# Kernel optimization log

Hardware: AMD Instinct MI355X
Metric: run time of the kernel (lower is better)

The kernel has to match this reference:

```python
import jax, jax.numpy as jnp
import numpy as np

N, KIN = 400000, 128
K = 64
RADIUS = 0.5
BIG = 1e9  # sentinel distance for invalid (nidx < 0) neighbours


def setup_inputs() -> dict:
    key = jax.random.key(0)
    k1, k2, k3 = jax.random.split(key, 3)
    distances = jax.random.uniform(k1, (N, KIN), dtype=jnp.float32)
    idx = jax.random.randint(k2, (N, KIN), 0, N, dtype=jnp.int32)
    neg = jax.random.uniform(k3, (N, KIN)) < 0.05
    nidx = jnp.where(neg, jnp.int32(-1), idx)
    return {"distances": distances, "nidx": nidx}


def reference(distances, nidx):
    # Push invalid neighbours to the end of the sort order
    tfdist = jnp.where(nidx < 0, jnp.float32(BIG), distances)
    # Per-row ascending sort by masked distance; only the first K are needed
    sorting = jnp.argsort(tfdist, axis=1)[:, :K]  # [N, K]
    snidx = jnp.take_along_axis(nidx, sorting, axis=1)       # [N, K]
    sdist = jnp.take_along_axis(distances, sorting, axis=1)  # [N, K]
    # Radius mask: drop neighbours beyond RADIUS
    beyond = sdist > RADIUS
    snidx = jnp.where(beyond, jnp.int32(-1), snidx)
    sdist = jnp.where(beyond, jnp.float32(0.0), sdist)
    return (sdist, snidx)
```

## Files before the change

kernel.cpp:

```cpp
#include <hip/hip_runtime.h>

#define N_ROWS 400000
#define KIN 128
#define KOUT 64
#define RPW 4
#define WPB 4

typedef unsigned int uint32;
typedef unsigned int v2u __attribute__((ext_vector_type(2)));


template <int CTRL>
__device__ __forceinline__ uint32 dpp32(uint32 k) {
    return (uint32)__builtin_amdgcn_update_dpp(0, (int)k, CTRL, 0xF, 0xF, true);
}
__device__ __forceinline__ uint32 x4swap(uint32 k) {
    uint32 o = (uint32)__builtin_amdgcn_update_dpp((int)k, (int)k, 0x104, 0xF, 0x5, true);
    o = (uint32)__builtin_amdgcn_update_dpp((int)o, (int)k, 0x114, 0xF, 0xA, true);
    return o;
}
__device__ __forceinline__ void pl32pair(uint32 k, uint32& A, uint32& B) {
    const v2u r = __builtin_amdgcn_permlane32_swap(k, k, false, false);
    A = r[0]; B = r[1];
}
#if __has_builtin(__builtin_amdgcn_permlane16_swap)
__device__ __forceinline__ void pl16pair(uint32 k, uint32& A, uint32& B) {
    const v2u r = __builtin_amdgcn_permlane16_swap(k, k, false, false);
    A = r[0]; B = r[1];
}
#else
__device__ __forceinline__ void pl16pair(uint32 k, uint32& A, uint32& B) {
    A = k; B = (uint32)__builtin_amdgcn_ds_swizzle((int)k, 0x401F);
}
#endif
__device__ __forceinline__ uint32 umin32(uint32 a, uint32 b) { return a < b ? a : b; }
__device__ __forceinline__ uint32 med3(uint32 a, uint32 b, uint32 m) {
    uint32 d;
    asm("v_med3_u32 %0, %1, %2, %3" : "=v"(d) : "v"(a), "v"(b), "v"(m));
    return d;
}

#define T_DPP(CTRL, M) { _Pragma("unroll") \
    for (int r_ = 0; r_ < RPW; ++r_) { \
        keyA[r_] = med3(keyA[r_], dpp32<CTRL>(keyA[r_]), M); \
        keyB[r_] = med3(keyB[r_], dpp32<CTRL>(keyB[r_]), M); } }

#define T_X4(M) { _Pragma("unroll") \
    for (int r_ = 0; r_ < RPW; ++r_) { \
        keyA[r_] = med3(keyA[r_], x4swap(keyA[r_]), M); \
        keyB[r_] = med3(keyB[r_], x4swap(keyB[r_]), M); } }

#define T_PL16(M) { _Pragma("unroll") \
    for (int r_ = 0; r_ < RPW; ++r_) { \
        uint32 A0, B0, A1, B1; \
        pl16pair(keyA[r_], A0, B0); pl16pair(keyB[r_], A1, B1); \
        keyA[r_] = med3(A0, B0, M); \
        keyB[r_] = med3(A1, B1, M); } }

#define T_PL32(M) { _Pragma("unroll") \
    for (int r_ = 0; r_ < RPW; ++r_) { \
        uint32 A0, B0, A1, B1; \
        pl32pair(keyA[r_], A0, B0); pl32pair(keyB[r_], A1, B1); \
        keyA[r_] = med3(A0, B0, M); \
        keyB[r_] = med3(A1, B1, M); } }

#define M_DPP(CTRL, M) { _Pragma("unroll") \
    for (int r_ = 0; r_ < RPW; ++r_) { \
        keyA[r_] = med3(keyA[r_], dpp32<CTRL>(keyA[r_]), M); } }
#define M_X4(M) { _Pragma("unroll") \
    for (int r_ = 0; r_ < RPW; ++r_) { \
        keyA[r_] = med3(keyA[r_], x4swap(keyA[r_]), M); } }
#define M_PL16(M) { _Pragma("unroll") \
    for (int r_ = 0; r_ < RPW; ++r_) { \
        uint32 A, B; pl16pair(keyA[r_], A, B); \
        keyA[r_] = med3(A, B, M); } }
#define M_PL32(M) { _Pragma("unroll") \
    for (int r_ = 0; r_ < RPW; ++r_) { \
        uint32 A, B; pl32pair(keyA[r_], A, B); \
        keyA[r_] = med3(A, B, M); } }

#define QP_X1 0xB1
#define QP_X2 0x4E
#define ROR8  0x128

__global__ __launch_bounds__(256) void SortAndSelectNeighbours_kernel(
    const float* __restrict__ distances,
    const int*   __restrict__ nidx,
    float*       __restrict__ out)
{
    __shared__ int s_nidx[WPB][RPW][KIN];

    const int lane = threadIdx.x & 63;
    const int wid  = threadIdx.x >> 6;
    const int row0 = (blockIdx.x * WPB + wid) * RPW;
    const int c0 = 2 * lane;

    float2 dv[RPW];
    int2   nv[RPW];
    #pragma unroll
    for (int r = 0; r < RPW; ++r) {
        const uint32 off = (uint32)(row0 + r) * KIN + (uint32)c0;
        dv[r] = *reinterpret_cast<const float2*>(distances + off);
        nv[r] = *reinterpret_cast<const int2*>(nidx + off);
    }

    uint32 keyA[RPW], keyB[RPW];
    #pragma unroll
    for (int r = 0; r < RPW; ++r) {
        *reinterpret_cast<int2*>(&s_nidx[wid][r][c0]) = nv[r];
        const uint32 k0 = (uint32)(dv[r].x * 16777216.0f);
        const uint32 k1 = (uint32)(dv[r].y * 16777216.0f);
        keyA[r] =  (((k0 << 7) | (uint32)c0)       | ((uint32)nv[r].x & 0x80000000u));
        keyB[r] = ~(((k1 << 7) | (uint32)(c0 + 1)) | ((uint32)nv[r].y & 0x80000000u));
    }

    const uint32 lm = (uint32)lane;
    const uint32 m0 = (uint32)-(int)(lm & 1u);
    const uint32 m1 = (uint32)-(int)((lm >> 1) & 1u);
    const uint32 m2 = (uint32)-(int)((lm >> 2) & 1u);
    const uint32 m3 = (uint32)-(int)((lm >> 3) & 1u);
    const uint32 m4 = (uint32)-(int)((lm >> 4) & 1u);
    const uint32 m5 = (uint32)-(int)((lm >> 5) & 1u);
    const uint32 g01 = m0 ^ m1;
    const uint32 g12 = m1 ^ m2, g02 = m0 ^ m2;
    const uint32 g23 = m2 ^ m3, g13 = m1 ^ m3, g03 = m0 ^ m3;
    const uint32 g34 = m3 ^ m4, g24 = m2 ^ m4, g14 = m1 ^ m4, g04 = m0 ^ m4;
    const uint32 g45 = m4 ^ m5, g35 = m3 ^ m5, g25 = m2 ^ m5, g15 = m1 ^ m5,
                 g05 = m0 ^ m5;

    T_DPP(QP_X1, g01);
    T_DPP(QP_X2, g12); T_DPP(QP_X1, g02);
    T_X4(g23); T_DPP(QP_X2, g13); T_DPP(QP_X1, g03);
    T_DPP(ROR8, g34); T_X4(g24); T_DPP(QP_X2, g14); T_DPP(QP_X1, g04);
    T_PL16(g45); T_DPP(ROR8, g35); T_X4(g25); T_DPP(QP_X2, g15);
    T_DPP(QP_X1, g05);
    T_PL32(m5); T_PL16(m4); T_DPP(ROR8, m3); T_X4(m2); T_DPP(QP_X2, m1);
    T_DPP(QP_X1, m0);

    #pragma unroll
    for (int r = 0; r < RPW; ++r)
        keyA[r] = umin32(keyA[r], ~keyB[r]);

    M_PL32(m5); M_PL16(m4); M_DPP(ROR8, m3); M_X4(m2); M_DPP(QP_X2, m1);
    M_DPP(QP_X1, m0);

    #pragma unroll
    for (int r = 0; r < RPW; ++r) {
        const bool bey = keyA[r] > 0x4000007Fu;
        const float d = (float)(keyA[r] >> 7) * 5.9604644775390625e-8f;
        const int col = (int)(keyA[r] & 127u);
        const int n   = s_nidx[wid][r][col];

        const uint32 od = (uint32)(row0 + r) * KOUT + (uint32)lane;
        out[od] = bey ? 0.0f : d;
        out[(uint32)(N_ROWS * KOUT) + od] = bey ? -1.0f : (float)n;
    }
}

extern "C" void kernel_launch(void* const* d_in, const int* in_sizes, int n_in,
                              void* d_out, int out_size, void* d_ws, size_t ws_size,
                              hipStream_t stream) {
    const float* distances = (const float*)d_in[0];
    const int*   nidx      = (const int*)d_in[1];
    float*       out       = (float*)d_out;

    dim3 grid(N_ROWS / (WPB * RPW));
    dim3 block(256);
    hipLaunchKernelGGL(SortAndSelectNeighbours_kernel, grid, block, 0, stream,
                       distances, nidx, out);
}
```

Before: 115.4 us.

## Use persistent grid-stride waves with register prefetch of next row group

Replaces the one-wave-per-row-group launch with a fixed grid of 2048 blocks whose waves loop over row groups in grid-stride fashion. The loads for the next group are issued before the sorting network runs on the current one, so memory latency overlaps the DPP/permlane compute. This removes per-block launch and setup overhead but doubles the registers held for input data and reduces the number of waves resident at once. Shared-memory reuse across iterations within a wave relies on wave-level lockstep ordering.

```diff
diff --git a/kernel.cpp b/kernel.cpp
--- a/kernel.cpp
+++ b/kernel.cpp
@@ -5,6 +5,9 @@
 #define KOUT 64
 #define RPW 4
 #define WPB 4
+#define G_BLOCKS 2048
+#define TOT_WAVES (G_BLOCKS * WPB)
+#define TOT_WB (N_ROWS / RPW)
 
 typedef unsigned int uint32;
 typedef unsigned int v2u __attribute__((ext_vector_type(2)));
@@ -44,26 +47,20 @@
     for (int r_ = 0; r_ < RPW; ++r_) { \
         keyA[r_] = med3(keyA[r_], dpp32<CTRL>(keyA[r_]), M); \
         keyB[r_] = med3(keyB[r_], dpp32<CTRL>(keyB[r_]), M); } }
-
 #define T_X4(M) { _Pragma("unroll") \
     for (int r_ = 0; r_ < RPW; ++r_) { \
         keyA[r_] = med3(keyA[r_], x4swap(keyA[r_]), M); \
         keyB[r_] = med3(keyB[r_], x4swap(keyB[r_]), M); } }
-
 #define T_PL16(M) { _Pragma("unroll") \
     for (int r_ = 0; r_ < RPW; ++r_) { \
         uint32 A0, B0, A1, B1; \
         pl16pair(keyA[r_], A0, B0); pl16pair(keyB[r_], A1, B1); \
-        keyA[r_] = med3(A0, B0, M); \
-        keyB[r_] = med3(A1, B1, M); } }
-
+        keyA[r_] = med3(A0, B0, M); keyB[r_] = med3(A1, B1, M); } }
 #define T_PL32(M) { _Pragma("unroll") \
     for (int r_ = 0; r_ < RPW; ++r_) { \
         uint32 A0, B0, A1, B1; \
         pl32pair(keyA[r_], A0, B0); pl32pair(keyB[r_], A1, B1); \
-        keyA[r_] = med3(A0, B0, M); \
-        keyB[r_] = med3(A1, B1, M); } }
-
+        keyA[r_] = med3(A0, B0, M); keyB[r_] = med3(A1, B1, M); } }
 #define M_DPP(CTRL, M) { _Pragma("unroll") \
     for (int r_ = 0; r_ < RPW; ++r_) { \
         keyA[r_] = med3(keyA[r_], dpp32<CTRL>(keyA[r_]), M); } }
@@ -72,12 +69,10 @@
         keyA[r_] = med3(keyA[r_], x4swap(keyA[r_]), M); } }
 #define M_PL16(M) { _Pragma("unroll") \
     for (int r_ = 0; r_ < RPW; ++r_) { \
-        uint32 A, B; pl16pair(keyA[r_], A, B); \
-        keyA[r_] = med3(A, B, M); } }
+        uint32 A, B; pl16pair(keyA[r_], A, B); keyA[r_] = med3(A, B, M); } }
 #define M_PL32(M) { _Pragma("unroll") \
     for (int r_ = 0; r_ < RPW; ++r_) { \
-        uint32 A, B; pl32pair(keyA[r_], A, B); \
-        keyA[r_] = med3(A, B, M); } }
+        uint32 A, B; pl32pair(keyA[r_], A, B); keyA[r_] = med3(A, B, M); } }
 
 #define QP_X1 0xB1
 #define QP_X2 0x4E
@@ -92,27 +87,8 @@
 
     const int lane = threadIdx.x & 63;
     const int wid  = threadIdx.x >> 6;
-    const int row0 = (blockIdx.x * WPB + wid) * RPW;
-    const int c0 = 2 * lane;
-
-    float2 dv[RPW];
-    int2   nv[RPW];
-    #pragma unroll
-    for (int r = 0; r < RPW; ++r) {
-        const uint32 off = (uint32)(row0 + r) * KIN + (uint32)c0;
-        dv[r] = *reinterpret_cast<const float2*>(distances + off);
-        nv[r] = *reinterpret_cast<const int2*>(nidx + off);
-    }
-
-    uint32 keyA[RPW], keyB[RPW];
-    #pragma unroll
-    for (int r = 0; r < RPW; ++r) {
-        *reinterpret_cast<int2*>(&s_nidx[wid][r][c0]) = nv[r];
-        const uint32 k0 = (uint32)(dv[r].x * 16777216.0f);
-        const uint32 k1 = (uint32)(dv[r].y * 16777216.0f);
-        keyA[r] =  (((k0 << 7) | (uint32)c0)       | ((uint32)nv[r].x & 0x80000000u));
-        keyB[r] = ~(((k1 << 7) | (uint32)(c0 + 1)) | ((uint32)nv[r].y & 0x80000000u));
-    }
+    const int c0   = 2 * lane;
+    const uint32 waveg = (uint32)blockIdx.x * WPB + (uint32)wid;
 
     const uint32 lm = (uint32)lane;
     const uint32 m0 = (uint32)-(int)(lm & 1u);
@@ -128,32 +104,69 @@
     const uint32 g45 = m4 ^ m5, g35 = m3 ^ m5, g25 = m2 ^ m5, g15 = m1 ^ m5,
                  g05 = m0 ^ m5;
 
-    T_DPP(QP_X1, g01);
-    T_DPP(QP_X2, g12); T_DPP(QP_X1, g02);
-    T_X4(g23); T_DPP(QP_X2, g13); T_DPP(QP_X1, g03);
-    T_DPP(ROR8, g34); T_X4(g24); T_DPP(QP_X2, g14); T_DPP(QP_X1, g04);
-    T_PL16(g45); T_DPP(ROR8, g35); T_X4(g25); T_DPP(QP_X2, g15);
-    T_DPP(QP_X1, g05);
-    T_PL32(m5); T_PL16(m4); T_DPP(ROR8, m3); T_X4(m2); T_DPP(QP_X2, m1);
-    T_DPP(QP_X1, m0);
-
-    #pragma unroll
-    for (int r = 0; r < RPW; ++r)
-        keyA[r] = umin32(keyA[r], ~keyB[r]);
-
-    M_PL32(m5); M_PL16(m4); M_DPP(ROR8, m3); M_X4(m2); M_DPP(QP_X2, m1);
-    M_DPP(QP_X1, m0);
-
+    uint32 wb = waveg;
+    float2 dv[RPW];
+    int2   nv[RPW];
     #pragma unroll
     for (int r = 0; r < RPW; ++r) {
-        const bool bey = keyA[r] > 0x4000007Fu;
-        const float d = (float)(keyA[r] >> 7) * 5.9604644775390625e-8f;
-        const int col = (int)(keyA[r] & 127u);
-        const int n   = s_nidx[wid][r][col];
+        const uint32 off = (wb * RPW + (uint32)r) * KIN + (uint32)c0;
+        dv[r] = *reinterpret_cast<const float2*>(distances + off);
+        nv[r] = *reinterpret_cast<const int2*>(nidx + off);
+    }
 
-        const uint32 od = (uint32)(row0 + r) * KOUT + (uint32)lane;
-        out[od] = bey ? 0.0f : d;
-        out[(uint32)(N_ROWS * KOUT) + od] = bey ? -1.0f : (float)n;
+    #pragma unroll 1
+    for (;;) {
+        uint32 keyA[RPW], keyB[RPW];
+        #pragma unroll
+        for (int r = 0; r < RPW; ++r) {
+            *reinterpret_cast<int2*>(&s_nidx[wid][r][c0]) = nv[r];
+            const uint32 k0 = (uint32)(dv[r].x * 16777216.0f);
+            const uint32 k1 = (uint32)(dv[r].y * 16777216.0f);
+            keyA[r] =  (((k0 << 7) | (uint32)c0)       | ((uint32)nv[r].x & 0x80000000u));
+            keyB[r] = ~(((k1 << 7) | (uint32)(c0 + 1)) | ((uint32)nv[r].y & 0x80000000u));
+        }
+
+        const uint32 wb_next = wb + TOT_WAVES;
+        const bool have_next = wb_next < TOT_WB;
+        if (have_next) {
+            #pragma unroll
+            for (int r = 0; r < RPW; ++r) {
+                const uint32 off = (wb_next * RPW + (uint32)r) * KIN + (uint32)c0;
+                dv[r] = *reinterpret_cast<const float2*>(distances + off);
+                nv[r] = *reinterpret_cast<const int2*>(nidx + off);
+            }
+        }
+
+        T_DPP(QP_X1, g01);
+        T_DPP(QP_X2, g12); T_DPP(QP_X1, g02);
+        T_X4(g23); T_DPP(QP_X2, g13); T_DPP(QP_X1, g03);
+        T_DPP(ROR8, g34); T_X4(g24); T_DPP(QP_X2, g14);
+        T_DPP(QP_X1, g04);
+        T_PL16(g45); T_DPP(ROR8, g35); T_X4(g25); T_DPP(QP_X2, g15);
+        T_DPP(QP_X1, g05);
+        T_PL32(m5); T_PL16(m4); T_DPP(ROR8, m3); T_X4(m2);
+        T_DPP(QP_X2, m1); T_DPP(QP_X1, m0);
+
+        #pragma unroll
+        for (int r = 0; r < RPW; ++r)
+            keyA[r] = umin32(keyA[r], ~keyB[r]);
+        M_PL32(m5); M_PL16(m4); M_DPP(ROR8, m3); M_X4(m2);
+        M_DPP(QP_X2, m1); M_DPP(QP_X1, m0);
+
+        #pragma unroll
+        for (int r = 0; r < RPW; ++r) {
+            const bool bey = keyA[r] > 0x4000007Fu;
+            const float d = (float)(keyA[r] >> 7) * 5.9604644775390625e-8f;
+            const int col = (int)(keyA[r] & 127u);
+            const int n   = s_nidx[wid][r][col];
+
+            const uint32 od = (wb * RPW + (uint32)r) * KOUT + (uint32)lane;
+            out[od] = bey ? 0.0f : d;
+            out[(uint32)(N_ROWS * KOUT) + od] = bey ? -1.0f : (float)n;
+        }
+
+        if (!have_next) break;
+        wb = wb_next;
     }
 }
 
@@ -164,7 +177,7 @@
     const int*   nidx      = (const int*)d_in[1];
     float*       out       = (float*)d_out;
 
-    dim3 grid(N_ROWS / (WPB * RPW));
+    dim3 grid(G_BLOCKS);
     dim3 block(256);
     hipLaunchKernelGGL(SortAndSelectNeighbours_kernel, grid, block, 0, stream,
                        distances, nidx, out);
```

Result: slower. 140.0 us (+21.3%).
